# Optimization experiments

Hardware: AMD Instinct MI355X
Metric: run time of the kernel (lower is better)

The kernel has to match this reference:

```python
import jax, jax.numpy as jnp
import numpy as np

P_DROP = 0.6  # dropout prob from the source module
N_NODES = 50000
N_EDGES = 800000


def _cheb_edge_weights(edge_index, num_nodes):
    # ChebConv with sym normalization and default lambda_max=2.0:
    # scaled Laplacian hat(L) = 2L/lambda_max - I = -D^{-1/2} A D^{-1/2}
    # (diagonal becomes 0), so edge weight = -1/sqrt(deg[row]*deg[col]).
    row, col = edge_index[0], edge_index[1]
    deg = jnp.zeros((num_nodes,), jnp.float32).at[row].add(1.0)
    dis = jnp.where(deg > 0, jax.lax.rsqrt(jnp.maximum(deg, 1.0)), 0.0)
    return -dis[row] * dis[col]


def _prop(x, row, col, w, n):
    # hat(L) @ x via gather-scale-scatter over the edge list
    return jnp.zeros((n, x.shape[1]), x.dtype).at[row].add(w[:, None] * x[col])


def _cheb_conv(x, row, col, w, W, b, n):
    # Chebyshev recursion: Tx0 = x, Tx1 = hat(L) x, Tx_k = 2 hat(L) Tx_{k-1} - Tx_{k-2}
    Tx0 = x
    out = Tx0 @ W[0]
    Tx1 = _prop(Tx0, row, col, w, n)
    out = out + Tx1 @ W[1]
    for k in range(2, W.shape[0]):
        Tx2 = 2.0 * _prop(Tx1, row, col, w, n) - Tx0
        out = out + Tx2 @ W[k]
        Tx0, Tx1 = Tx1, Tx2
    return out + b


def _dropout(x, key, p):
    keep = jax.random.bernoulli(key, 1.0 - p, x.shape)
    return jnp.where(keep, x * (1.0 / (1.0 - p)), 0.0)


def setup_inputs() -> dict:
    key = jax.random.key(0)
    ks = jax.random.split(key, 8)
    x = jax.random.normal(ks[0], (N_NODES, 64), jnp.float32)
    edge_index = jax.random.randint(ks[1], (2, N_EDGES), 0, N_NODES, jnp.int64)
    W0 = jax.random.normal(ks[2], (2, 64, 64), jnp.float32) * 0.1
    b0 = jnp.zeros((64,), jnp.float32)
    W1 = jax.random.normal(ks[3], (2, 64, 64), jnp.float32) * 0.1
    b1 = jnp.zeros((64,), jnp.float32)
    W2 = jax.random.normal(ks[4], (2, 64, 32), jnp.float32) * 0.1
    b2 = jnp.zeros((32,), jnp.float32)
    return {"x": x, "edge_index": edge_index, "W0": W0, "b0": b0,
            "W1": W1, "b1": b1, "W2": W2, "b2": b2}


def reference(x, edge_index, W0, b0, W1, b1, W2, b2):
    row, col = edge_index[0], edge_index[1]
    n = x.shape[0]
    w = _cheb_edge_weights(edge_index, n)
    dkey = jax.random.key(1)
    params = [(W0, b0), (W1, b1), (W2, b2)]
    for i, (W, b) in enumerate(params):
        x = _dropout(x, jax.random.fold_in(dkey, i), P_DROP)
        x = _cheb_conv(x, row, col, w, W, b, n)
        if i < len(params) - 1:
            x = jax.nn.relu(x)
    return x
```

## Files before the change

kernel.cpp:

```cpp
#include <hip/hip_runtime.h>
#include <stdint.h>

typedef _Float16 half8 __attribute__((ext_vector_type(8)));
typedef float float4v __attribute__((ext_vector_type(4)));

__host__ __device__ inline void tf2x32(uint32_t k0, uint32_t k1,
                                       uint32_t x0, uint32_t x1,
                                       uint32_t* o0, uint32_t* o1) {
  const uint32_t ks2 = k0 ^ k1 ^ 0x1BD11BDAu;
#define ROTL(v, s) (((v) << (s)) | ((v) >> (32 - (s))))
#define RND(r) do { x0 += x1; x1 = ROTL(x1, r); x1 ^= x0; } while (0)
  x0 += k0; x1 += k1;
  RND(13); RND(15); RND(26); RND(6);
  x0 += k1; x1 += ks2 + 1u;
  RND(17); RND(29); RND(16); RND(24);
  x0 += ks2; x1 += k0 + 2u;
  RND(13); RND(15); RND(26); RND(6);
  x0 += k0; x1 += k1 + 3u;
  RND(17); RND(29); RND(16); RND(24);
  x0 += k1; x1 += ks2 + 4u;
  RND(13); RND(15); RND(26); RND(6);
  x0 += ks2; x1 += k0 + 5u;
  *o0 = x0; *o1 = x1;
#undef RND
#undef ROTL
}

__device__ inline bool drop_keep(uint32_t k0, uint32_t k1, uint32_t idx) {
  uint32_t o0, o1;
  tf2x32(k0, k1, 0u, idx, &o0, &o1);
  uint32_t bits = o0 ^ o1;
  float u = __uint_as_float((bits >> 9) | 0x3f800000u) - 1.0f;
  return u < 0.4f;
}

__global__ void k_fill2(const int* __restrict__ row, const int* __restrict__ col,
                        int* __restrict__ cnt, uint16_t* __restrict__ cs,
                        int e, int rows_per_xcd) {
  const int owner = blockIdx.x & 7;
  const int i = (blockIdx.x >> 3) * 256 + threadIdx.x;
  if (i < e) {
    int r = row[i];
    if (r / rows_per_xcd == owner) {
      int pos = atomicAdd(&cnt[r], 1);
      if (pos < 64) cs[(r << 6) + pos] = (uint16_t)col[i];
    }
  }
}

__global__ void k_drop(const float* __restrict__ x, const int* __restrict__ cnt,
                       uint16_t* __restrict__ cs, float* __restrict__ dis,
                       _Float16* __restrict__ y, _Float16* __restrict__ ys,
                       _Float16* __restrict__ ysb, uint32_t k0, uint32_t k1,
                       int n, int nd,
                       const float* __restrict__ W0, const float* __restrict__ W1,
                       const float* __restrict__ W2, _Float16* __restrict__ wh) {
  int i = blockIdx.x * 256 + threadIdx.x;
  if (i < 20480) {
    int d = i;
    if (d < 8192) {
      int o = d >> 7, k = d & 127;
      wh[d] = (_Float16)W0[k * 64 + o];
    } else if (d < 16384) {
      int d1 = d - 8192, o = d1 >> 7, k = d1 & 127;
      wh[d] = (_Float16)W1[k * 64 + o];
    } else {
      int d2 = d - 16384, o = d2 >> 7, k = d2 & 127;
      wh[d] = (_Float16)W2[k * 32 + o];
    }
  }
  if (i < 64) {
    ys[((size_t)n << 6) + i]  = (_Float16)0.f;
    ysb[((size_t)n << 6) + i] = (_Float16)0.f;
  }
  if (i < nd) {
    const int r = i >> 6;
    const int t = i & 63;
    const int d = cnt[r];
    const float dis_r = (d > 0) ? rsqrtf((float)d) : 0.0f;
    float v = drop_keep(k0, k1, (uint32_t)i) ? x[i] * 2.5f : 0.0f;
    y[i]  = (_Float16)v;
    ys[i] = (_Float16)(dis_r * v);
    if (t == 0) dis[r] = dis_r;
    const int cn = d < 64 ? d : 64;
    const int rnd = (cn + 7) & ~7;
    if (t >= cn && t < rnd) cs[(r << 6) + t] = (uint16_t)n;
  }
}

template<int T>
__device__ __forceinline__ void gatherT(int idx_all, int rnd, int jb, int g,
                                        int sub,
                                        const _Float16* __restrict__ ysg,
                                        uint32_t dummy, float acc[8]) {
  half8 hv[T];
  #pragma unroll
  for (int j = 0; j < T; ++j) {
    int sh = __shfl(idx_all, (jb + j) * 8 + g, 64);
    uint32_t c = ((jb + j) * 8 < rnd) ? (uint32_t)(sh & 0xffff) : dummy;
    hv[j] = *(const half8*)((const char*)ysg + (c << 7) + (sub << 4));
  }
  #pragma unroll
  for (int j = 0; j < T; ++j)
    #pragma unroll
    for (int k = 0; k < 8; ++k) acc[k] += (float)hv[j][k];
}

template<int COUT, bool RELU, bool DROPN, bool WBF>
__global__ __launch_bounds__(256, 8) void k_conv(
    const _Float16* __restrict__ yg, const _Float16* __restrict__ ysg,
    const int* __restrict__ cnt, const uint16_t* __restrict__ cs,
    const float* __restrict__ dis, const _Float16* __restrict__ wt,
    const float* __restrict__ b, float* __restrict__ outf,
    _Float16* __restrict__ outb, _Float16* __restrict__ outs,
    uint32_t nk0, uint32_t nk1, int n) {
  constexpr int R  = 16;
  constexpr int TS = 136;
  __shared__ __align__(16) _Float16 xp[R][TS];

  const int wave = threadIdx.x >> 6;
  const int t    = threadIdx.x & 63;
  const int row0 = blockIdx.x * R;
  const int g    = t >> 3;
  const int sub  = t & 7;
  const uint32_t dummy = (uint32_t)n;

  int      idxs[4], ds4[4];
  float    dv4[4];
  _Float16 ygv[4];
  #pragma unroll
  for (int i = 0; i < 4; ++i) {
    int r = row0 + wave * 4 + i;
    r = r < n ? r : n - 1;
    idxs[i] = cs[(r << 6) + t];
    ds4[i]  = cnt[r];
    dv4[i]  = dis[r];
    ygv[i]  = yg[(uint32_t)(r << 6) + t];
  }

  #pragma unroll
  for (int i = 0; i < 4; ++i) {
    const int cn  = ds4[i] < 64 ? ds4[i] : 64;
    const int rnd = (cn + 7) & ~7;
    float acc[8] = {0.f, 0.f, 0.f, 0.f, 0.f, 0.f, 0.f, 0.f};
    if (rnd <= 16) {
      gatherT<2>(idxs[i], rnd, 0, g, sub, ysg, dummy, acc);
    } else if (rnd <= 32) {
      gatherT<4>(idxs[i], rnd, 0, g, sub, ysg, dummy, acc);
    } else {
      gatherT<4>(idxs[i], rnd, 0, g, sub, ysg, dummy, acc);
      gatherT<4>(idxs[i], rnd, 4, g, sub, ysg, dummy, acc);
    }

    const bool b0 = (g & 1), b1 = (g & 2), b2 = (g & 4);
    float a4[4], a2[2], v;
    #pragma unroll
    for (int m = 0; m < 4; ++m) {
      float keep = b0 ? acc[2 * m + 1] : acc[2 * m];
      float send = b0 ? acc[2 * m]     : acc[2 * m + 1];
      a4[m] = keep + __shfl_xor(send, 8, 64);
    }
    #pragma unroll
    for (int m = 0; m < 2; ++m) {
      float keep = b1 ? a4[2 * m + 1] : a4[2 * m];
      float send = b1 ? a4[2 * m]     : a4[2 * m + 1];
      a2[m] = keep + __shfl_xor(send, 16, 64);
    }
    {
      float keep = b2 ? a2[1] : a2[0];
      float send = b2 ? a2[0] : a2[1];
      v = keep + __shfl_xor(send, 32, 64);
    }
    const int rl = wave * 4 + i;
    xp[rl][t]                    = ygv[i];
    xp[rl][64 + (sub * 8 + g)]   = (_Float16)(-dv4[i] * v);
  }
  __syncthreads();

  constexpr int NW = COUT / 16;
  const int nn   = t & 15;
  const int quad = t >> 4;
  if (wave < NW) {
    const int colg = wave * 16 + nn;
    float4v acc = {0.f, 0.f, 0.f, 0.f};
    #pragma unroll
    for (int ks = 0; ks < 4; ++ks) {
      half8 a  = *(const half8*)&xp[nn][quad * 8 + 32 * ks];
      half8 bb = *(const half8*)&wt[(size_t)colg * 128 + quad * 8 + 32 * ks];
      acc = __builtin_amdgcn_mfma_f32_16x16x32_f16(a, bb, acc, 0, 0, 0);
    }
    const float bias = b[colg];
    #pragma unroll
    for (int rg = 0; rg < 4; ++rg) {
      const int rl = quad * 4 + rg;
      const int rr = row0 + rl;
      if (rr < n) {
        float v = acc[rg] + bias;
        if (RELU) v = fmaxf(v, 0.0f);
        if (DROPN) {
          if (drop_keep(nk0, nk1, (uint32_t)(rr * 64 + colg))) v *= 2.5f;
          else v = 0.0f;
        }
        if (WBF) {
          outb[(size_t)rr * COUT + colg] = (_Float16)v;
          outs[(size_t)rr * COUT + colg] = (_Float16)(dis[rr] * v);
        } else {
          outf[(size_t)rr * COUT + colg] = v;
        }
      }
    }
  }
}

extern "C" void kernel_launch(void* const* d_in, const int* in_sizes, int n_in,
                              void* d_out, int out_size, void* d_ws, size_t ws_size,
                              hipStream_t stream) {
  const float* x   = (const float*)d_in[0];
  const int*   ei  = (const int*)d_in[1];
  const float* W0  = (const float*)d_in[2];
  const float* b0  = (const float*)d_in[3];
  const float* W1f = (const float*)d_in[4];
  const float* b1  = (const float*)d_in[5];
  const float* W2  = (const float*)d_in[6];
  const float* b2  = (const float*)d_in[7];
  float* out = (float*)d_out;

  const int n = in_sizes[0] / 64;
  const int e = in_sizes[1] / 2;
  const int* row = ei;
  const int* col = ei + e;

  size_t off = 0;
  auto carve = [&](size_t elems) {
    size_t o = off;
    off += (elems + 255) & ~(size_t)255;
    return o;
  };
  int* base = (int*)d_ws;
  int*      cnt = base + carve(n);
  float*    dis = (float*)(base + carve(n));
  uint16_t* cs  = (uint16_t*)(base + carve((size_t)n * 32));
  _Float16* ya  = (_Float16*)(base + carve((size_t)n * 32));
  _Float16* ysa = (_Float16*)(base + carve((size_t)(n + 1) * 32));
  _Float16* yb  = (_Float16*)(base + carve((size_t)n * 32));
  _Float16* ysb = (_Float16*)(base + carve((size_t)(n + 1) * 32));
  _Float16* wh  = (_Float16*)(base + carve(10240));
  (void)ws_size;
  _Float16* wh0 = wh;
  _Float16* wh1 = wh + 8192;
  _Float16* wh2 = wh + 16384;

  uint32_t dk[3][2];
  for (uint32_t i = 0; i < 3; ++i) tf2x32(0u, 1u, 0u, i, &dk[i][0], &dk[i][1]);

  hipMemsetAsync(cnt, 0, (size_t)n * 4, stream);

  const int nchunk = (e + 255) / 256;
  const int bd = ((n * 64) + 255) / 256;
  const int bc = (n + 15) / 16;
  const int rpx = (n + 7) / 8;

  k_fill2<<<nchunk * 8, 256, 0, stream>>>(row, col, cnt, cs, e, rpx);
  k_drop<<<bd, 256, 0, stream>>>(x, cnt, cs, dis, ya, ysa, ysb,
                                 dk[0][0], dk[0][1], n, n * 64,
                                 W0, W1f, W2, wh);

  k_conv<64, true,  true,  true ><<<bc, 256, 0, stream>>>(
      ya, ysa, cnt, cs, dis, wh0, b0, nullptr, yb, ysb, dk[1][0], dk[1][1], n);
  k_conv<64, true,  true,  true ><<<bc, 256, 0, stream>>>(
      yb, ysb, cnt, cs, dis, wh1, b1, nullptr, ya, ysa, dk[2][0], dk[2][1], n);
  k_conv<32, false, false, false><<<bc, 256, 0, stream>>>(
      ya, ysa, cnt, cs, dis, wh2, b2, out, nullptr, nullptr, 0u, 0u, n);
}
```

Before: 197.5 us.

## Batch neighbor gathers for all four rows before accumulating to raise memory parallelism

Issues the first 32 neighbor gathers for each of a wave's four rows up front, with a scheduling barrier, before any accumulation. This lets more loads be in flight at once instead of serialising gather-then-reduce per row. The degree-based 2/4-load specialisation is dropped, so low-degree rows now always issue four loads, some of them redundant dummy loads. The launch-bounds occupancy hint drops from 8 to 4 to make room for the extra registers, and the yg value is now written straight into shared memory.

```diff
diff --git a/kernel.cpp b/kernel.cpp
--- a/kernel.cpp
+++ b/kernel.cpp
@@ -88,26 +88,27 @@
   }
 }
 
-template<int T>
-__device__ __forceinline__ void gatherT(int idx_all, int rnd, int jb, int g,
-                                        int sub,
-                                        const _Float16* __restrict__ ysg,
-                                        uint32_t dummy, float acc[8]) {
-  half8 hv[T];
-  #pragma unroll
-  for (int j = 0; j < T; ++j) {
+__device__ __forceinline__ void issue4(int idx_all, int rnd, int jb, int g,
+                                       int sub,
+                                       const _Float16* __restrict__ ysg,
+                                       uint32_t dummy, half8 hv[4]) {
+  #pragma unroll
+  for (int j = 0; j < 4; ++j) {
     int sh = __shfl(idx_all, (jb + j) * 8 + g, 64);
     uint32_t c = ((jb + j) * 8 < rnd) ? (uint32_t)(sh & 0xffff) : dummy;
     hv[j] = *(const half8*)((const char*)ysg + (c << 7) + (sub << 4));
   }
-  #pragma unroll
-  for (int j = 0; j < T; ++j)
+}
+
+__device__ __forceinline__ void consume4(const half8 hv[4], float acc[8]) {
+  #pragma unroll
+  for (int j = 0; j < 4; ++j)
     #pragma unroll
     for (int k = 0; k < 8; ++k) acc[k] += (float)hv[j][k];
 }
 
 template<int COUT, bool RELU, bool DROPN, bool WBF>
-__global__ __launch_bounds__(256, 8) void k_conv(
+__global__ __launch_bounds__(256, 4) void k_conv(
     const _Float16* __restrict__ yg, const _Float16* __restrict__ ysg,
     const int* __restrict__ cnt, const uint16_t* __restrict__ cs,
     const float* __restrict__ dis, const _Float16* __restrict__ wt,
@@ -125,31 +126,35 @@
   const int sub  = t & 7;
   const uint32_t dummy = (uint32_t)n;
 
-  int      idxs[4], ds4[4];
+  int      idxs[4], rnd4[4];
   float    dv4[4];
-  _Float16 ygv[4];
   #pragma unroll
   for (int i = 0; i < 4; ++i) {
     int r = row0 + wave * 4 + i;
     r = r < n ? r : n - 1;
     idxs[i] = cs[(r << 6) + t];
-    ds4[i]  = cnt[r];
+    const int d = cnt[r];
     dv4[i]  = dis[r];
-    ygv[i]  = yg[(uint32_t)(r << 6) + t];
-  }
+    const int cn = d < 64 ? d : 64;
+    rnd4[i] = (cn + 7) & ~7;
+    xp[wave * 4 + i][t] = yg[(uint32_t)(r << 6) + t];
+  }
+
+  half8 hv0[4], hv1[4], hv2[4], hv3[4];
+  issue4(idxs[0], rnd4[0], 0, g, sub, ysg, dummy, hv0);
+  issue4(idxs[1], rnd4[1], 0, g, sub, ysg, dummy, hv1);
+  issue4(idxs[2], rnd4[2], 0, g, sub, ysg, dummy, hv2);
+  issue4(idxs[3], rnd4[3], 0, g, sub, ysg, dummy, hv3);
+  __builtin_amdgcn_sched_barrier(0);
 
   #pragma unroll
   for (int i = 0; i < 4; ++i) {
-    const int cn  = ds4[i] < 64 ? ds4[i] : 64;
-    const int rnd = (cn + 7) & ~7;
+    half8* hv = (i == 0) ? hv0 : (i == 1) ? hv1 : (i == 2) ? hv2 : hv3;
     float acc[8] = {0.f, 0.f, 0.f, 0.f, 0.f, 0.f, 0.f, 0.f};
-    if (rnd <= 16) {
-      gatherT<2>(idxs[i], rnd, 0, g, sub, ysg, dummy, acc);
-    } else if (rnd <= 32) {
-      gatherT<4>(idxs[i], rnd, 0, g, sub, ysg, dummy, acc);
-    } else {
-      gatherT<4>(idxs[i], rnd, 0, g, sub, ysg, dummy, acc);
-      gatherT<4>(idxs[i], rnd, 4, g, sub, ysg, dummy, acc);
+    consume4(hv, acc);
+    if (rnd4[i] > 32) {
+      issue4(idxs[i], rnd4[i], 4, g, sub, ysg, dummy, hv);
+      consume4(hv, acc);
     }
 
     const bool b0 = (g & 1), b1 = (g & 2), b2 = (g & 4);
@@ -171,9 +176,7 @@
       float send = b2 ? a2[0] : a2[1];
       v = keep + __shfl_xor(send, 32, 64);
     }
-    const int rl = wave * 4 + i;
-    xp[rl][t]                    = ygv[i];
-    xp[rl][64 + (sub * 8 + g)]   = (_Float16)(-dv4[i] * v);
+    xp[wave * 4 + i][64 + (sub * 8 + g)] = (_Float16)(-dv4[i] * v);
   }
   __syncthreads();
 
```

Measured after the change: 192.6 us. 1.03x faster.
